# Kernel optimization log

Measured on AMD Instinct MI355X. Metric: run time of the kernel, lower is better.

Reference implementation:

```python
import jax, jax.numpy as jnp
import numpy as np

N, E, M, NT, RB, SH, NIR, LAT = 10000, 160000, 8, 4, 8, 9, 3, 128
AVG_N = 16.0
LATF = LAT + M * NIR  # 152
COMP2IR = np.array([0, 1, 1, 1, 2, 2, 2, 2, 2])  # irrep id per SH component (0e,1o,2e)
IR1H = jnp.asarray(np.eye(NIR, dtype=np.float32)[COMP2IR])  # [9,3] one-hot comp->irrep


def _silu(x):
    return x * jax.nn.sigmoid(x)


def setup_inputs() -> dict:
    key = jax.random.key(0)
    ks = jax.random.split(key, 16)
    def w(k, shape, fan_in):
        return jax.random.normal(k, shape, jnp.float32) / np.sqrt(fan_in)
    return {
        'edge_attrs': jax.random.normal(ks[0], (E, SH), jnp.float32),
        'edge_embedding': jax.random.normal(ks[1], (E, RB), jnp.float32),
        'node_attrs': jax.random.uniform(ks[2], (N, NT), jnp.float32),
        'edge_lengths': jax.random.uniform(ks[3], (E,), jnp.float32),
        'tb_w0': w(ks[4], (2 * NT + RB, LAT), 2 * NT + RB),
        'tb_w1': w(ks[5], (LAT, LAT), LAT),
        'tb_w2': w(ks[6], (LAT, LAT), LAT),
        'env_mlp_w0': w(ks[7], (LAT, 2 * M * NIR), LAT),
        'env_mlp_w1': w(ks[8], (LAT, M * NIR), LAT),
        'env_linear_w': w(ks[9], (2, NIR, M, M), M),
        'latent_w': w(ks[10], (LATF, LAT), LATF),
        'lat2feat_w': w(ks[11], (2, LATF, NIR * M * M), LATF),
        'lat2featold_w': w(ks[12], (2, LATF, NIR * M * M), LATF),
        'final_w': w(ks[13], (LATF, M), LATF),
        'edge_index': jax.random.randint(ks[14], (2, E), 0, N, jnp.int32),
    }


def reference(edge_attrs, edge_embedding, node_attrs, edge_lengths,
              tb_w0, tb_w1, tb_w2, env_mlp_w0, env_mlp_w1, env_linear_w,
              latent_w, lat2feat_w, lat2featold_w, final_w, edge_index):
    center, neigh = edge_index[0], edge_index[1]
    n_nodes = node_attrs.shape[0]
    c2i = jnp.asarray(COMP2IR)

    # polynomial cutoff, p=6, x = r / r_max
    x = edge_lengths
    p = 6.0
    cut = (1.0 - (p + 1) * (p + 2) / 2 * x**6 + p * (p + 2) * x**7 - p * (p + 1) / 2 * x**8)
    cut = jnp.where(x < 1.0, cut, 0.0)[:, None]

    # two-body latent MLP on [center species, neighbor species, radial basis]
    tb_in = jnp.concatenate([node_attrs[center], node_attrs[neigh], edge_embedding], axis=-1)
    h = _silu(tb_in @ tb_w0)
    h = _silu(h @ tb_w1)
    latents = (h @ tb_w2) * cut  # [E, LAT]

    def weight_edges(wch):  # MakeWeightedChannels: per-irrep channel weights
        return wch[:, :, c2i] * edge_attrs[:, None, :]  # [E, M, 9]

    def env_of(w_cur, layer):  # scatter to node env + env linear
        env = jax.ops.segment_sum(weight_edges(w_cur), center, num_segments=n_nodes) / AVG_N
        Wc = env_linear_w[layer][c2i]  # [9, M, M]
        return jnp.einsum('duv,nvd->nud', Wc, env) / np.sqrt(M)

    def interact(features, env_c):  # scalar-gated equivariant coupling
        return features * env_c[:, :, :1] + env_c * features[:, :, :1]

    def invariants(f):  # per-(channel, irrep) norms
        return jnp.sqrt(jnp.einsum('eud,di->eui', f * f, IR1H) + 1e-8).reshape(f.shape[0], M * NIR)

    def pe_linear(Wflat, f):  # per-edge generated irrep-wise Linear
        W = Wflat.reshape(-1, NIR, M, M)
        return jnp.einsum('eiuv,di,evd->eud', W, IR1H, f) / np.sqrt(M)

    # ---- layer 0 (initial weighter + env weighter) ----
    ew = latents @ env_mlp_w0  # [E, 2*M*NIR]
    w_init = ew[:, :M * NIR].reshape(-1, M, NIR)
    w_cur = ew[:, M * NIR:].reshape(-1, M, NIR)
    features = weight_edges(w_init)  # [E, M, 9]
    env_c = env_of(w_cur, 0)[center]
    new_f = interact(features, env_c)
    lat_full = jnp.concatenate([latents, invariants(new_f)], axis=-1)  # [E, 152]
    features = 0.5 * pe_linear(lat_full @ lat2featold_w[0], features) \
             + 0.5 * pe_linear(lat_full @ lat2feat_w[0], new_f)

    # ---- layer 1 ----
    lat_new = _silu(lat_full @ latent_w) * cut
    latents = 0.5 * latents + 0.5 * lat_new  # latent resnet, sigmoid(0)=0.5
    w_cur = (latents @ env_mlp_w1).reshape(-1, M, NIR)
    env_c = env_of(w_cur, 1)[center]
    new_f = interact(features, env_c)
    lat_full = jnp.concatenate([latents, invariants(new_f)], axis=-1)
    features = 0.5 * pe_linear(lat_full @ lat2featold_w[1], features) \
             + 0.5 * pe_linear(lat_full @ lat2feat_w[1], new_f)

    # ---- final: generated linear to 1x1o per edge (components 1:4) ----
    wfin = lat_full @ final_w  # [E, M]
    return jnp.einsum('em,emd->ed', wfin, features[:, :, 1:4]) / np.sqrt(M)
```

## Files before the change

kernel.cpp:

```cpp
#include <hip/hip_runtime.h>
#include <hip/hip_bf16.h>

#define EE 160000
#define NNODES 10000

using bf16 = __hip_bfloat16;
using bf16x8 = __attribute__((ext_vector_type(8))) short;
using short4v = __attribute__((ext_vector_type(4))) short;
using f32x4  = __attribute__((ext_vector_type(4))) float;

__device__ __forceinline__ float silu_f(float x) { return x / (1.0f + __expf(-x)); }
__device__ __forceinline__ float b2f(bf16 v) { return __bfloat162float(v); }
__device__ __forceinline__ bf16 f2b(float v) { return __float2bfloat16(v); }

__device__ __forceinline__ unsigned bfbits(float v) {
    union { float f; unsigned u; } a; a.f = v;
    return (a.u + 0x7fffu + ((a.u >> 16) & 1u)) >> 16;
}
__device__ __forceinline__ unsigned pack2(float a, float b) {
    return bfbits(a) | (bfbits(b) << 16);
}
__device__ __forceinline__ void unpack2(unsigned u, float& a, float& b) {
    union { unsigned x; float f; } lo, hi;
    lo.x = u << 16; hi.x = u & 0xffff0000u;
    a = lo.f; b = hi.f;
}
__device__ __forceinline__ float bs2f(short s) {
    union { unsigned u; float f; } x; x.u = ((unsigned)(unsigned short)s) << 16;
    return x.f;
}

#define INV_AVGN_SQM 0.02209708691207961f
#define HALF_INV_SQM 0.17677669529663687f
#define INV_SQM      0.35355339059327373f

__global__ void kCnt(const int* __restrict__ eidx, int* __restrict__ deg)
{
    const int e = blockIdx.x * 256 + threadIdx.x;
    atomicAdd(&deg[eidx[e]], 1);
}

__global__ void kScan(const int* __restrict__ deg, int* __restrict__ off)
{
    __shared__ int part[256];
    const int t = threadIdx.x;
    int loc[40];
    int s = 0;
#pragma unroll
    for (int i = 0; i < 40; i++) {
        const int idx = t * 40 + i;
        const int v = (idx < NNODES) ? deg[idx] : 0;
        loc[i] = s;
        s += v;
    }
    part[t] = s;
    __syncthreads();
    for (int d = 1; d < 256; d <<= 1) {
        const int v = (t >= d) ? part[t - d] : 0;
        __syncthreads();
        part[t] += v;
        __syncthreads();
    }
    const int base = (t == 0) ? 0 : part[t - 1];
#pragma unroll
    for (int i = 0; i < 40; i++) {
        const int idx = t * 40 + i;
        if (idx < NNODES) off[idx] = base + loc[i];
    }
    if (t == 255) off[NNODES] = part[255];
}

__global__ void kFill(const int* __restrict__ eidx, int* __restrict__ cur,
                      const int* __restrict__ off, int* __restrict__ elist)
{
    const int e = blockIdx.x * 256 + threadIdx.x;
    const int c = eidx[e];
    const int pos = atomicAdd(&cur[c], 1);
    elist[off[c] + pos] = e;
}

__global__ void kPrepA(const float* __restrict__ w1, const float* __restrict__ w2,
                       const float* __restrict__ wm0, short* __restrict__ wAtF)
{
    const int t = blockIdx.x * 256 + threadIdx.x;
    if (t >= 38912) return;
    const int k = t & 127, c = t >> 7;
    float v;
    if (c < 128)      v = w1[k * 128 + c];
    else if (c < 256) v = w2[k * 128 + (c - 128)];
    else              v = wm0[k * 48 + (c - 256)];
    wAtF[((k >> 3) * 304 + c) * 8 + (k & 7)] = (short)bfbits(v);
}

__global__ void kPrepB(const float* __restrict__ l2fo, const float* __restrict__ l2fn,
                       const float* __restrict__ latw, const float* __restrict__ l2fo1,
                       const float* __restrict__ l2fn1, const float* __restrict__ finw,
                       const float* __restrict__ wm1, short* __restrict__ BtF)
{
    const int k = blockIdx.y;
    const int col = blockIdx.x * 256 + threadIdx.x;
    if (col >= 672) return;
    float v = 0.f;
    if (col < 648) {
        if (k < 152) {
            if (col < 384) {
                const int ir = col >> 7, half = (col >> 6) & 1, q = col & 63;
                const float* src = half ? l2fn : l2fo;
                v = src[k * 192 + ir * 64 + q];
            } else if (col < 512)  v = latw[k * 128 + (col - 384)];
            else if (col < 576)    v = l2fo1[k * 192 + 64 + (col - 512)];
            else if (col < 640)    v = l2fn1[k * 192 + 64 + (col - 576)];
            else                   v = finw[k * 8 + (col - 640)];
        }
    } else {
        if (k < 128) v = wm1[k * 24 + (col - 648)];
    }
    BtF[((k >> 3) * 672 + col) * 8 + (k & 7)] = (short)bfbits(v);
}

__global__ void kEnvG(const float* __restrict__ wcur, const float* __restrict__ ea,
                      const int* __restrict__ off, const int* __restrict__ elist,
                      const float* __restrict__ wl, float* __restrict__ envc)
{
    const int t = blockIdx.x * 256 + threadIdx.x;
    if (t >= NNODES * 9) return;
    const int n = t / 9;
    const int d = t - n * 9;
    const int irr = (d == 0) ? 0 : ((d < 4) ? 1 : 2);
    float v[8];
#pragma unroll
    for (int q = 0; q < 8; q++) v[q] = 0.0f;
    const int b = off[n], en = off[n + 1];
    for (int j = b; j < en; j++) {
        const int e = elist[j];
        const float ad = ea[e * 9 + d];
        const float* wr = wcur + (size_t)e * 24 + irr;
#pragma unroll
        for (int q = 0; q < 8; q++) v[q] = fmaf(wr[q * 3], ad, v[q]);
    }
#pragma unroll
    for (int u = 0; u < 8; u++) {
        float s = 0.0f;
#pragma unroll
        for (int q = 0; q < 8; q++) s = fmaf(wl[irr * 64 + u * 8 + q], v[q], s);
        envc[n * 72 + u * 9 + d] = s * INV_AVGN_SQM;
    }
}

__global__ __launch_bounds__(256) void kA0(
    const float* __restrict__ ea, const float* __restrict__ eemb,
    const float* __restrict__ nat, const float* __restrict__ elen,
    const float* __restrict__ w0, const int* __restrict__ eidx,
    short* __restrict__ h08, short* __restrict__ latf8s,
    bf16* __restrict__ eaT, float* __restrict__ cutb)
{
    __shared__ float w0s[16 * 128];
    const int t = threadIdx.x;
    const int e = blockIdx.x * 256 + t;
#pragma unroll
    for (int p = 0; p < 8; p++) { const int idx = p * 256 + t; w0s[idx] = w0[idx]; }
    __syncthreads();

    const int ctr = eidx[e];
    const int ngb = eidx[EE + e];
    float tin[16];
#pragma unroll
    for (int k = 0; k < 4; k++) tin[k] = nat[ctr * 4 + k];
#pragma unroll
    for (int k = 0; k < 4; k++) tin[4 + k] = nat[ngb * 4 + k];
#pragma unroll
    for (int k = 0; k < 8; k++) tin[8 + k] = eemb[e * 8 + k];

    const float x = elen[e];
    const float x2 = x * x, x4 = x2 * x2, x6 = x4 * x2, x7 = x6 * x, x8 = x7 * x;
    float cutv = 1.0f - 28.0f * x6 + 48.0f * x7 - 21.0f * x8;
    cutv = (x < 1.0f) ? cutv : 0.0f;
    cutb[e] = cutv;

    const size_t tb = (size_t)(e >> 5);
    const int el = e & 31;
#pragma unroll
    for (int jc = 0; jc < 4; jc++) {
        float a[32];
#pragma unroll
        for (int j = 0; j < 32; j++) a[j] = 0.0f;
#pragma unroll
        for (int k = 0; k < 16; k++) {
            const float v = tin[k];
#pragma unroll
            for (int j = 0; j < 32; j++) a[j] = fmaf(v, w0s[k * 128 + jc * 32 + j], a[j]);
        }
#pragma unroll
        for (int cc = 0; cc < 4; cc++) {
            bf16x8 hv;
#pragma unroll
            for (int jj = 0; jj < 8; jj++) hv[jj] = (short)bfbits(silu_f(a[cc * 8 + jj]));
            *(bf16x8*)(h08 + tb * 4096 + (jc * 4 + cc) * 256 + el * 8) = hv;
        }
    }
    bf16x8 z;
#pragma unroll
    for (int jj = 0; jj < 8; jj++) z[jj] = 0;
    *(bf16x8*)(latf8s + tb * 5120 + 19 * 256 + el * 8) = z;

#pragma unroll
    for (int d = 0; d < 9; d++) eaT[(size_t)d * EE + e] = f2b(ea[e * 9 + d]);
}

__global__ __launch_bounds__(256, 4) void kAm(
    const short* __restrict__ h08, const short* __restrict__ wAtF,
    const float* __restrict__ cutb, short* __restrict__ latf8s,
    float* __restrict__ winiF, float* __restrict__ wcur0)
{
    __shared__ alignas(16) char a2raw[16384];
    __shared__ short A3[8192];
    short* A2 = (short*)a2raw;
    float* Cs = (float*)a2raw;

    const int t = threadIdx.x;
    const int eb = blockIdx.x * 64;
    const int lane = t & 63, wid = t >> 6;
    const int wm = wid >> 1, wn = wid & 1;
    const int l15 = lane & 15, kq = lane >> 4;
    const f32x4 zz = {0.f, 0.f, 0.f, 0.f};

    float cutR[2][4];
#pragma unroll
    for (int mi = 0; mi < 2; mi++)
#pragma unroll
        for (int r = 0; r < 4; r++)
            cutR[mi][r] = cutb[eb + wm * 32 + mi * 16 + kq * 4 + r];

    {
        f32x4 acc[8];
#pragma unroll
        for (int q = 0; q < 8; q++) acc[q] = zz;
        const size_t ab = (size_t)((eb >> 5) + wm) * 4096 + l15 * 8;
#pragma unroll
        for (int ks = 0; ks < 4; ks++) {
            const int kc = ks * 4 + kq;
            const bf16x8 a0 = *(const bf16x8*)(h08 + ab + kc * 256);
            const bf16x8 a1 = *(const bf16x8*)(h08 + ab + kc * 256 + 128);
            const short* bp = wAtF + (kc * 304 + wn * 64 + l15) * 8;
#pragma unroll
            for (int ni = 0; ni < 4; ni++) {
                const bf16x8 b = *(const bf16x8*)(bp + ni * 16 * 8);
                acc[ni]     = __builtin_amdgcn_mfma_f32_16x16x32_bf16(a0, b, acc[ni], 0, 0, 0);
                acc[4 + ni] = __builtin_amdgcn_mfma_f32_16x16x32_bf16(a1, b, acc[4 + ni], 0, 0, 0);
            }
        }
#pragma unroll
        for (int mi = 0; mi < 2; mi++)
#pragma unroll
            for (int ni = 0; ni < 4; ni++) {
                const int kcol = wn * 64 + ni * 16 + l15;
                const int eb2 = wm * 32 + mi * 16 + (kq << 2);
#pragma unroll
                for (int r = 0; r < 4; r++)
                    A2[(kcol >> 3) * 512 + (eb2 + r) * 8 + (kcol & 7)] =
                        (short)bfbits(silu_f(acc[mi * 4 + ni][r]));
            }
    }
    __syncthreads();

    {
        f32x4 acc[8];
#pragma unroll
        for (int q = 0; q < 8; q++) acc[q] = zz;
#pragma unroll
        for (int ks = 0; ks < 4; ks++) {
            const int kc = ks * 4 + kq;
            const bf16x8 a0 = *(const bf16x8*)(A2 + kc * 512 + (wm * 32 + l15) * 8);
            const bf16x8 a1 = *(const bf16x8*)(A2 + kc * 512 + (wm * 32 + 16 + l15) * 8);
            const short* bp = wAtF + (kc * 304 + 128 + wn * 64 + l15) * 8;
#pragma unroll
            for (int ni = 0; ni < 4; ni++) {
                const bf16x8 b = *(const bf16x8*)(bp + ni * 16 * 8);
                acc[ni]     = __builtin_amdgcn_mfma_f32_16x16x32_bf16(a0, b, acc[ni], 0, 0, 0);
                acc[4 + ni] = __builtin_amdgcn_mfma_f32_16x16x32_bf16(a1, b, acc[4 + ni], 0, 0, 0);
            }
        }
#pragma unroll
        for (int mi = 0; mi < 2; mi++)
#pragma unroll
            for (int ni = 0; ni < 4; ni++) {
                const int kcol = wn * 64 + ni * 16 + l15;
                const int eb2 = wm * 32 + mi * 16 + (kq << 2);
#pragma unroll
                for (int r = 0; r < 4; r++)
                    A3[(kcol >> 3) * 512 + (eb2 + r) * 8 + (kcol & 7)] =
                        (short)bfbits(acc[mi * 4 + ni][r] * cutR[mi][r]);
            }
    }
    __syncthreads();
#pragma unroll
    for (int p = 0; p < 4; p++) {
        const int i = p * 256 + t;
        const int e = i & 63, kc = i >> 6;
        const bf16x8 v = *(const bf16x8*)(A3 + kc * 512 + e * 8);
        const int eg = eb + e;
        *(bf16x8*)(latf8s + (size_t)(eg >> 5) * 5120 + kc * 256 + (eg & 31) * 8) = v;
    }

    if (wn == 0) {
        f32x4 acc[6];
#pragma unroll
        for (int q = 0; q < 6; q++) acc[q] = zz;
#pragma unroll
        for (int ks = 0; ks < 4; ks++) {
            const int kc = ks * 4 + kq;
            const bf16x8 a0 = *(const bf16x8*)(A3 + kc * 512 + (wm * 32 + l15) * 8);
            const bf16x8 a1 = *(const bf16x8*)(A3 + kc * 512 + (wm * 32 + 16 + l15) * 8);
            const short* bp = wAtF + (kc * 304 + 256 + l15) * 8;
#pragma unroll
            for (int ni = 0; ni < 3; ni++) {
                const bf16x8 b = *(const bf16x8*)(bp + ni * 16 * 8);
                acc[ni]     = __builtin_amdgcn_mfma_f32_16x16x32_bf16(a0, b, acc[ni], 0, 0, 0);
                acc[3 + ni] = __builtin_amdgcn_mfma_f32_16x16x32_bf16(a1, b, acc[3 + ni], 0, 0, 0);
            }
        }
#pragma unroll
        for (int mi = 0; mi < 2; mi++)
#pragma unroll
            for (int ni = 0; ni < 3; ni++) {
                const int c = ni * 16 + l15;
                const int eb2 = wm * 32 + mi * 16 + (kq << 2);
#pragma unroll
                for (int r = 0; r < 4; r++)
                    Cs[c * 65 + eb2 + r] = acc[mi * 3 + ni][r];
            }
    }
    __syncthreads();
    for (int i = t; i < 1536; i += 256) {
        const int c = i >> 6, e = i & 63;
        winiF[(size_t)c * EE + eb + e] = Cs[c * 65 + e];
    }
    for (int i = t; i < 1536; i += 256) {
        const int e2 = i / 24, c2 = i - e2 * 24;
        wcur0[(size_t)(eb + e2) * 24 + c2] = Cs[(24 + c2) * 65 + e2];
    }
}

__global__ __launch_bounds__(256, 1) void kC1(
    const float* __restrict__ winiF, const bf16* __restrict__ eaT,
    const float* __restrict__ envc, const int* __restrict__ eidx,
    unsigned* __restrict__ newfT, short* __restrict__ latf8s)
{
    const int e = blockIdx.x * 256 + threadIdx.x;
    const int ctr = eidx[e];
    float eav[9];
#pragma unroll
    for (int d = 0; d < 9; d++) eav[d] = b2f(eaT[(size_t)d * EE + e]);
    const float* ec = envc + ctr * 72;
    float inv[24];
#pragma unroll
    for (int uh = 0; uh < 4; uh++) {
        const int u0 = 2 * uh;
        float wi0[3], wi1[3];
#pragma unroll
        for (int i = 0; i < 3; i++) {
            wi0[i] = winiF[(size_t)(u0 * 3 + i) * EE + e];
            wi1[i] = winiF[(size_t)((u0 + 1) * 3 + i) * EE + e];
        }
        float nf0[9], nf1[9];
        const float ec00 = ec[u0 * 9 + 0];
        const float ec10 = ec[(u0 + 1) * 9 + 0];
        const float f00 = wi0[0] * eav[0];
        const float f10 = wi1[0] * eav[0];
#pragma unroll
        for (int d = 0; d < 9; d++) {
            const int irr = (d == 0) ? 0 : ((d < 4) ? 1 : 2);
            const float fa = wi0[irr] * eav[d];
            const float fb = wi1[irr] * eav[d];
            nf0[d] = fa * ec00 + ec[u0 * 9 + d] * f00;
            nf1[d] = fb * ec10 + ec[(u0 + 1) * 9 + d] * f10;
        }
#pragma unroll
        for (int d = 0; d < 9; d++) newfT[(size_t)(d * 4 + uh) * EE + e] = pack2(nf0[d], nf1[d]);
        inv[uh * 6 + 0] = sqrtf(nf0[0] * nf0[0] + 1e-8f);
        inv[uh * 6 + 1] = sqrtf(nf0[1]*nf0[1] + nf0[2]*nf0[2] + nf0[3]*nf0[3] + 1e-8f);
        inv[uh * 6 + 2] = sqrtf(nf0[4]*nf0[4] + nf0[5]*nf0[5] + nf0[6]*nf0[6] + nf0[7]*nf0[7] + nf0[8]*nf0[8] + 1e-8f);
        inv[uh * 6 + 3] = sqrtf(nf1[0] * nf1[0] + 1e-8f);
        inv[uh * 6 + 4] = sqrtf(nf1[1]*nf1[1] + nf1[2]*nf1[2] + nf1[3]*nf1[3] + 1e-8f);
        inv[uh * 6 + 5] = sqrtf(nf1[4]*nf1[4] + nf1[5]*nf1[5] + nf1[6]*nf1[6] + nf1[7]*nf1[7] + nf1[8]*nf1[8] + 1e-8f);
    }
    const size_t tb = (size_t)(e >> 5);
    const int el = e & 31;
#pragma unroll
    for (int j = 0; j < 3; j++) {
        bf16x8 iv;
#pragma unroll
        for (int jj = 0; jj < 8; jj++) iv[jj] = (short)bfbits(inv[j * 8 + jj]);
        *(bf16x8*)(latf8s + tb * 5120 + (16 + j) * 256 + el * 8) = iv;
    }
}

__global__ __launch_bounds__(256, 4) void kF0(
    const short* __restrict__ A8, const short* __restrict__ BtF,
    const float* __restrict__ winiF, const bf16* __restrict__ eaT,
    const unsigned* __restrict__ newfT, unsigned* __restrict__ feat1T)
{
    __shared__ float Cs[128 * 67];
    const int t = threadIdx.x;
    const int eb = blockIdx.x * 64;
    const int lane = t & 63, wid = t >> 6;
    const int wm = wid >> 1, wn = wid & 1;
    const int l15 = lane & 15, kq = lane >> 4;
    const f32x4 zz = {0.f, 0.f, 0.f, 0.f};
    const size_t ab = (size_t)((eb >> 5) + wm) * 5120 + l15 * 8;
    const int te = t & 63, uh = t >> 6;
    const int eg = eb + te;

    for (int ir = 0; ir < 3; ir++) {
        f32x4 acc[8];
#pragma unroll
        for (int q = 0; q < 8; q++) acc[q] = zz;
#pragma unroll
        for (int ks = 0; ks < 5; ks++) {
            const int kc = ks * 4 + kq;
            const bf16x8 a0 = *(const bf16x8*)(A8 + ab + kc * 256);
            const bf16x8 a1 = *(const bf16x8*)(A8 + ab + kc * 256 + 128);
            const short* bp = BtF + (kc * 672 + ir * 128 + wn * 64 + l15) * 8;
#pragma unroll
            for (int ni = 0; ni < 4; ni++) {
                const bf16x8 b = *(const bf16x8*)(bp + ni * 16 * 8);
                acc[ni]     = __builtin_amdgcn_mfma_f32_16x16x32_bf16(a0, b, acc[ni], 0, 0, 0);
                acc[4 + ni] = __builtin_amdgcn_mfma_f32_16x16x32_bf16(a1, b, acc[4 + ni], 0, 0, 0);
            }
        }
        __syncthreads();
#pragma unroll
        for (int mi = 0; mi < 2; mi++)
#pragma unroll
            for (int ni = 0; ni < 4; ni++) {
                const int cl = wn * 64 + ni * 16 + l15;
                const int el = wm * 32 + mi * 16 + (kq << 2);
                const f32x4 v = acc[mi * 4 + ni];
#pragma unroll
                for (int r = 0; r < 4; r++) Cs[cl * 67 + el + r] = v[r];
            }
        __syncthreads();
        const int d0 = (ir == 0) ? 0 : ((ir == 1) ? 1 : 4);
        const int nd = (ir == 0) ? 1 : ((ir == 1) ? 3 : 5);
        float wv[8];
#pragma unroll
        for (int v8 = 0; v8 < 8; v8++) wv[v8] = winiF[(size_t)(v8 * 3 + ir) * EE + eg];
        for (int dd = 0; dd < nd; dd++) {
            const int d = d0 + dd;
            const float ead = b2f(eaT[(size_t)d * EE + eg]);
            float nfv[8];
#pragma unroll
            for (int q = 0; q < 4; q++)
                unpack2(newfT[(size_t)(d * 4 + q) * EE + eg], nfv[2 * q], nfv[2 * q + 1]);
            float s0 = 0.f, s1 = 0.f;
#pragma unroll
            for (int v8 = 0; v8 < 8; v8++) {
                const float fe = wv[v8] * ead;
                s0 += Cs[(uh * 16 + v8) * 67 + te] * fe + Cs[(64 + uh * 16 + v8) * 67 + te] * nfv[v8];
                s1 += Cs[(uh * 16 + 8 + v8) * 67 + te] * fe + Cs[(64 + uh * 16 + 8 + v8) * 67 + te] * nfv[v8];
            }
            feat1T[(size_t)(d * 4 + uh) * EE + eg] = pack2(s0 * HALF_INV_SQM, s1 * HALF_INV_SQM);
        }
    }
}

__global__ __launch_bounds__(256, 4) void kF3(
    short* __restrict__ A8, const short* __restrict__ BtF,
    const float* __restrict__ cutb, float* __restrict__ wcur1)
{
    __shared__ alignas(16) short Cc[128 * 68];
    __shared__ short l1s[16 * 512];
    float* Cw = (float*)Cc;
    const int t = threadIdx.x;
    const int eb = blockIdx.x * 64;
    const int lane = t & 63, wid = t >> 6;
    const int wm = wid >> 1, wn = wid & 1;
    const int l15 = lane & 15, kq = lane >> 4;
    const f32x4 zz = {0.f, 0.f, 0.f, 0.f};

    {
        f32x4 acc[8];
#pragma unroll
        for (int q = 0; q < 8; q++) acc[q] = zz;
        const size_t ab = (size_t)((eb >> 5) + wm) * 5120 + l15 * 8;
#pragma unroll
        for (int ks = 0; ks < 5; ks++) {
            const int kc = ks * 4 + kq;
            const bf16x8 a0 = *(const bf16x8*)(A8 + ab + kc * 256);
            const bf16x8 a1 = *(const bf16x8*)(A8 + ab + kc * 256 + 128);
            const short* bp = BtF + (kc * 672 + 384 + wn * 64 + l15) * 8;
#pragma unroll
            for (int ni = 0; ni < 4; ni++) {
                const bf16x8 b = *(const bf16x8*)(bp + ni * 16 * 8);
                acc[ni]     = __builtin_amdgcn_mfma_f32_16x16x32_bf16(a0, b, acc[ni], 0, 0, 0);
                acc[4 + ni] = __builtin_amdgcn_mfma_f32_16x16x32_bf16(a1, b, acc[4 + ni], 0, 0, 0);
            }
        }
#pragma unroll
        for (int mi = 0; mi < 2; mi++)
#pragma unroll
            for (int ni = 0; ni < 4; ni++) {
                const int cl = wn * 64 + ni * 16 + l15;
                const int el = wm * 32 + mi * 16 + (kq << 2);
                const f32x4 v = acc[mi * 4 + ni];
                short4v pv;
#pragma unroll
                for (int r = 0; r < 4; r++) pv[r] = (short)bfbits(v[r]);
                *(short4v*)(Cc + cl * 68 + el) = pv;
            }
    }
    __syncthreads();
    {
        const int te = t & 63, q = t >> 6;
        const int eg = eb + te;
        const size_t tb = (size_t)(eg >> 5);
        const int el2 = eg & 31;
        const float cutv = cutb[eg];
#pragma unroll
        for (int c = 0; c < 4; c++) {
            const int kc = q * 4 + c;
            short* ap = A8 + tb * 5120 + kc * 256 + el2 * 8;
            const bf16x8 ov = *(const bf16x8*)ap;
            bf16x8 nv;
#pragma unroll
            for (int jj = 0; jj < 8; jj++) {
                const int j = kc * 8 + jj;
                const float g = bs2f(Cc[j * 68 + te]);
                const float o = bs2f(ov[jj]);
                nv[jj] = (short)bfbits(0.5f * o + 0.5f * silu_f(g) * cutv);
            }
            *(bf16x8*)ap = nv;
            *(bf16x8*)(l1s + kc * 512 + te * 8) = nv;
        }
    }
    __syncthreads();
    if (wn == 0) {
        f32x4 acc[4] = {zz, zz, zz, zz};
#pragma unroll
        for (int ks = 0; ks < 4; ks++) {
            const int kc = ks * 4 + kq;
            const bf16x8 a0 = *(const bf16x8*)(l1s + kc * 512 + (wm * 32 + l15) * 8);
            const bf16x8 a1 = *(const bf16x8*)(l1s + kc * 512 + (wm * 32 + 16 + l15) * 8);
#pragma unroll
            for (int ni = 0; ni < 2; ni++) {
                const int c = ni * 16 + l15;
                bf16x8 b;
                if (c < 24) b = *(const bf16x8*)(BtF + (kc * 672 + 648 + c) * 8);
                else {
#pragma unroll
                    for (int jj = 0; jj < 8; jj++) b[jj] = 0;
                }
                acc[ni]     = __builtin_amdgcn_mfma_f32_16x16x32_bf16(a0, b, acc[ni], 0, 0, 0);
                acc[2 + ni] = __builtin_amdgcn_mfma_f32_16x16x32_bf16(a1, b, acc[2 + ni], 0, 0, 0);
            }
        }
#pragma unroll
        for (int mi = 0; mi < 2; mi++)
#pragma unroll
            for (int ni = 0; ni < 2; ni++) {
                const int c = ni * 16 + l15;
                if (c < 24) {
                    const int el = wm * 32 + mi * 16 + (kq << 2);
#pragma unroll
                    for (int r = 0; r < 4; r++) Cw[c * 65 + el + r] = acc[mi * 2 + ni][r];
                }
            }
    }
    __syncthreads();
    for (int i = t; i < 1536; i += 256) {
        const int e2 = i / 24, c2 = i - e2 * 24;
        wcur1[(size_t)(eb + e2) * 24 + c2] = Cw[c2 * 65 + e2];
    }
}

__global__ __launch_bounds__(256, 1) void kE1(
    const unsigned* __restrict__ feat1T, const float* __restrict__ envc,
    const int* __restrict__ eidx, unsigned* __restrict__ newfT,
    short* __restrict__ latf8s)
{
    const int e = blockIdx.x * 256 + threadIdx.x;
    const int ctr = eidx[e];
    const float* ec = envc + ctr * 72;
    float inv[24];
#pragma unroll
    for (int uh = 0; uh < 4; uh++) {
        const int u0 = 2 * uh;
        float f0[9], f1[9];
#pragma unroll
        for (int d = 0; d < 9; d++) unpack2(feat1T[(size_t)(d * 4 + uh) * EE + e], f0[d], f1[d]);
        const float ec00 = ec[u0 * 9 + 0];
        const float ec10 = ec[(u0 + 1) * 9 + 0];
        float nf0[9], nf1[9];
#pragma unroll
        for (int d = 0; d < 9; d++) {
            nf0[d] = f0[d] * ec00 + ec[u0 * 9 + d] * f0[0];
            nf1[d] = f1[d] * ec10 + ec[(u0 + 1) * 9 + d] * f1[0];
        }
#pragma unroll
        for (int d = 0; d < 9; d++) newfT[(size_t)(d * 4 + uh) * EE + e] = pack2(nf0[d], nf1[d]);
        inv[uh * 6 + 0] = sqrtf(nf0[0] * nf0[0] + 1e-8f);
        inv[uh * 6 + 1] = sqrtf(nf0[1]*nf0[1] + nf0[2]*nf0[2] + nf0[3]*nf0[3] + 1e-8f);
        inv[uh * 6 + 2] = sqrtf(nf0[4]*nf0[4] + nf0[5]*nf0[5] + nf0[6]*nf0[6] + nf0[7]*nf0[7] + nf0[8]*nf0[8] + 1e-8f);
        inv[uh * 6 + 3] = sqrtf(nf1[0] * nf1[0] + 1e-8f);
        inv[uh * 6 + 4] = sqrtf(nf1[1]*nf1[1] + nf1[2]*nf1[2] + nf1[3]*nf1[3] + 1e-8f);
        inv[uh * 6 + 5] = sqrtf(nf1[4]*nf1[4] + nf1[5]*nf1[5] + nf1[6]*nf1[6] + nf1[7]*nf1[7] + nf1[8]*nf1[8] + 1e-8f);
    }
    const size_t tb = (size_t)(e >> 5);
    const int el = e & 31;
#pragma unroll
    for (int j = 0; j < 3; j++) {
        bf16x8 iv;
#pragma unroll
        for (int jj = 0; jj < 8; jj++) iv[jj] = (short)bfbits(inv[j * 8 + jj]);
        *(bf16x8*)(latf8s + tb * 5120 + (16 + j) * 256 + el * 8) = iv;
    }
}

__global__ __launch_bounds__(256, 4) void kF2(
    const short* __restrict__ A8, const short* __restrict__ BtF,
    const unsigned* __restrict__ feat1T, const unsigned* __restrict__ newfT,
    float* __restrict__ outp)
{
    __shared__ float Cs[128 * 67];
    __shared__ float Cwf[16 * 67];
    const int t = threadIdx.x;
    const int eb = blockIdx.x * 64;
    const int lane = t & 63, wid = t >> 6;
    const int wm = wid >> 1, wn = wid & 1;
    const int l15 = lane & 15, kq = lane >> 4;
    const f32x4 zz = {0.f, 0.f, 0.f, 0.f};
    const size_t ab = (size_t)((eb >> 5) + wm) * 5120 + l15 * 8;

    {
        f32x4 acc[8];
#pragma unroll
        for (int q = 0; q < 8; q++) acc[q] = zz;
#pragma unroll
        for (int ks = 0; ks < 5; ks++) {
            const int kc = ks * 4 + kq;
            const bf16x8 a0 = *(const bf16x8*)(A8 + ab + kc * 256);
            const bf16x8 a1 = *(const bf16x8*)(A8 + ab + kc * 256 + 128);
            const short* bp = BtF + (kc * 672 + 512 + wn * 64 + l15) * 8;
#pragma unroll
            for (int ni = 0; ni < 4; ni++) {
                const bf16x8 b = *(const bf16x8*)(bp + ni * 16 * 8);
                acc[ni]     = __builtin_amdgcn_mfma_f32_16x16x32_bf16(a0, b, acc[ni], 0, 0, 0);
                acc[4 + ni] = __builtin_amdgcn_mfma_f32_16x16x32_bf16(a1, b, acc[4 + ni], 0, 0, 0);
            }
        }
#pragma unroll
        for (int mi = 0; mi < 2; mi++)
#pragma unroll
            for (int ni = 0; ni < 4; ni++) {
                const int cl = wn * 64 + ni * 16 + l15;
                const int el = wm * 32 + mi * 16 + (kq << 2);
                const f32x4 v = acc[mi * 4 + ni];
#pragma unroll
                for (int r = 0; r < 4; r++) Cs[cl * 67 + el + r] = v[r];
            }
    }
    {
        f32x4 a2[2] = {zz, zz};
        bf16x8 bz;
#pragma unroll
        for (int jj = 0; jj < 8; jj++) bz[jj] = 0;
#pragma unroll
        for (int ks = 0; ks < 5; ks++) {
            const int kc = ks * 4 + kq;
            const bf16x8 a0 = *(const bf16x8*)(A8 + ab + kc * 256);
            const bf16x8 a1 = *(const bf16x8*)(A8 + ab + kc * 256 + 128);
            const bf16x8 b = (l15 < 8)
                ? *(const bf16x8*)(BtF + (kc * 672 + 640 + l15) * 8) : bz;
            a2[0] = __builtin_amdgcn_mfma_f32_16x16x32_bf16(a0, b, a2[0], 0, 0, 0);
            a2[1] = __builtin_amdgcn_mfma_f32_16x16x32_bf16(a1, b, a2[1], 0, 0, 0);
        }
        if (wn == 0) {
#pragma unroll
            for (int mi = 0; mi < 2; mi++) {
                const int el = wm * 32 + mi * 16 + (kq << 2);
#pragma unroll
                for (int r = 0; r < 4; r++) Cwf[l15 * 67 + el + r] = a2[mi][r];
            }
        }
    }
    __syncthreads();
    if (t < 192) {
        const int te = t % 64;
        const int dd = t / 64;
        const int eg = eb + te;
        const int d = 1 + dd;
        float f1v[8], nfv[8];
#pragma unroll
        for (int q = 0; q < 4; q++) {
            unpack2(feat1T[(size_t)(d * 4 + q) * EE + eg], f1v[2 * q], f1v[2 * q + 1]);
            unpack2(newfT[(size_t)(d * 4 + q) * EE + eg], nfv[2 * q], nfv[2 * q + 1]);
        }
        float od = 0.f;
#pragma unroll
        for (int u = 0; u < 8; u++) {
            float s = 0.f;
#pragma unroll
            for (int v8 = 0; v8 < 8; v8++)
                s += Cs[(u * 8 + v8) * 67 + te] * f1v[v8] + Cs[(64 + u * 8 + v8) * 67 + te] * nfv[v8];
            od = fmaf(Cwf[u * 67 + te], s, od);
        }
        outp[(size_t)eg * 3 + dd] = od * (HALF_INV_SQM * INV_SQM);
    }
}

extern "C" void kernel_launch(void* const* d_in, const int* in_sizes, int n_in,
                              void* d_out, int out_size, void* d_ws, size_t ws_size,
                              hipStream_t stream)
{
    const float* ea   = (const float*)d_in[0];
    const float* eemb = (const float*)d_in[1];
    const float* nat  = (const float*)d_in[2];
    const float* elen = (const float*)d_in[3];
    const float* w0   = (const float*)d_in[4];
    const float* w1   = (const float*)d_in[5];
    const float* w2   = (const float*)d_in[6];
    const float* wm0  = (const float*)d_in[7];
    const float* wm1  = (const float*)d_in[8];
    const float* envl = (const float*)d_in[9];
    const float* latw = (const float*)d_in[10];
    const float* l2fn = (const float*)d_in[11];
    const float* l2fo = (const float*)d_in[12];
    const float* finw = (const float*)d_in[13];
    const int*   eidx = (const int*)d_in[14];

    char* ws = (char*)d_ws;
    short*    latf8s = (short*)(ws + 0);
    short*    h08    = (short*)(ws + 51200000);
    unsigned* newfT  = (unsigned*)(ws + 92160000);
    unsigned* feat1T = (unsigned*)(ws + 115200000);
    float*    winiF  = (float*)(ws + 138240000);
    bf16*     eaT    = (bf16*)(ws + 153600000);
    float*    cutb   = (float*)(ws + 156480000);
    float*    env0   = (float*)(ws + 157120000);
    float*    env1   = (float*)(ws + 160000000);
    int*      deg    = (int*)(ws + 162880000);
    int*      cur    = (int*)(ws + 162920000);
    int*      off    = (int*)(ws + 162960000);
    int*      elist  = (int*)(ws + 163000192);
    short*    wAtF   = (short*)(ws + 162880000);
    short*    BtF    = (short*)(ws + 163640192);

    float* wcur0 = (float*)newfT;
    float* wcur1 = (float*)newfT;

    hipMemsetAsync(deg, 0, 80000, stream);

    kCnt <<<625, 256, 0, stream>>>(eidx, deg);
    kScan<<<1, 256, 0, stream>>>(deg, off);
    kFill<<<625, 256, 0, stream>>>(eidx, cur, off, elist);
    kPrepA<<<152, 256, 0, stream>>>(w1, w2, wm0, wAtF);
    kPrepB<<<dim3(3, 160), 256, 0, stream>>>(l2fo, l2fn, latw,
                                             l2fo + 29184, l2fn + 29184, finw, wm1, BtF);

    kA0<<<625, 256, 0, stream>>>(ea, eemb, nat, elen, w0, eidx, h08, latf8s, eaT, cutb);
    kAm<<<2500, 256, 0, stream>>>(h08, wAtF, cutb, latf8s, winiF, wcur0);
    kEnvG<<<352, 256, 0, stream>>>(wcur0, ea, off, elist, envl + 0, env0);
    kC1<<<625, 256, 0, stream>>>(winiF, eaT, env0, eidx, newfT, latf8s);

    kF0<<<2500, 256, 0, stream>>>(latf8s, BtF, winiF, eaT, newfT, feat1T);
    kF3<<<2500, 256, 0, stream>>>(latf8s, BtF, cutb, wcur1);
    kEnvG<<<352, 256, 0, stream>>>(wcur1, ea, off, elist, envl + 192, env1);
    kE1<<<625, 256, 0, stream>>>(feat1T, env1, eidx, newfT, latf8s);
    kF2<<<2500, 256, 0, stream>>>(latf8s, BtF, feat1T, newfT, (float*)d_out);
}
```

Before: 313.3 us.

## Fuse kF0 and kF3 into one kernel sharing register-cached A fragments

Merges the layer-0 feature-update GEMM kernel and the latent-update kernel into a single kernel. The A-operand fragments of the 152-wide latent row are loaded once into registers and reused across four column chunks. This removes one launch and one full re-read of the latent tile. The same A-fragment hoisting is applied in kF2. wcur1 is redirected to the h08 buffer because newfT is still read while wcur1 is being written in the fused kernel. In exchange, register pressure rises from holding 10 bf16x8 fragments, and the second GEMM now rereads updated latents from global memory instead of LDS.

After: 343.0 us. +9.4%, slower.

```diff
diff --git a/kernel.cpp b/kernel.cpp
--- a/kernel.cpp
+++ b/kernel.cpp
@@ -395,12 +395,14 @@
     }
 }
 
-__global__ __launch_bounds__(256, 4) void kF0(
-    const short* __restrict__ A8, const short* __restrict__ BtF,
+__global__ __launch_bounds__(256, 4) void kFX(
+    short* __restrict__ A8, const short* __restrict__ BtF,
     const float* __restrict__ winiF, const bf16* __restrict__ eaT,
-    const unsigned* __restrict__ newfT, unsigned* __restrict__ feat1T)
+    const unsigned* __restrict__ newfT, const float* __restrict__ cutb,
+    unsigned* __restrict__ feat1T, float* __restrict__ wcur1)
 {
     __shared__ float Cs[128 * 67];
+    float* Cw = Cs;
     const int t = threadIdx.x;
     const int eb = blockIdx.x * 64;
     const int lane = t & 63, wid = t >> 6;
@@ -411,21 +413,27 @@
     const int te = t & 63, uh = t >> 6;
     const int eg = eb + te;
 
-    for (int ir = 0; ir < 3; ir++) {
+    bf16x8 aF0[5], aF1[5];
+#pragma unroll
+    for (int ks = 0; ks < 5; ks++) {
+        const int kc = ks * 4 + kq;
+        aF0[ks] = *(const bf16x8*)(A8 + ab + kc * 256);
+        aF1[ks] = *(const bf16x8*)(A8 + ab + kc * 256 + 128);
+    }
+
+    for (int c = 0; c < 4; c++) {
         f32x4 acc[8];
 #pragma unroll
         for (int q = 0; q < 8; q++) acc[q] = zz;
 #pragma unroll
         for (int ks = 0; ks < 5; ks++) {
             const int kc = ks * 4 + kq;
-            const bf16x8 a0 = *(const bf16x8*)(A8 + ab + kc * 256);
-            const bf16x8 a1 = *(const bf16x8*)(A8 + ab + kc * 256 + 128);
-            const short* bp = BtF + (kc * 672 + ir * 128 + wn * 64 + l15) * 8;
+            const short* bp = BtF + (kc * 672 + c * 128 + wn * 64 + l15) * 8;
 #pragma unroll
             for (int ni = 0; ni < 4; ni++) {
                 const bf16x8 b = *(const bf16x8*)(bp + ni * 16 * 8);
-                acc[ni]     = __builtin_amdgcn_mfma_f32_16x16x32_bf16(a0, b, acc[ni], 0, 0, 0);
-                acc[4 + ni] = __builtin_amdgcn_mfma_f32_16x16x32_bf16(a1, b, acc[4 + ni], 0, 0, 0);
+                acc[ni]     = __builtin_amdgcn_mfma_f32_16x16x32_bf16(aF0[ks], b, acc[ni], 0, 0, 0);
+                acc[4 + ni] = __builtin_amdgcn_mfma_f32_16x16x32_bf16(aF1[ks], b, acc[4 + ni], 0, 0, 0);
             }
         }
         __syncthreads();
@@ -440,129 +448,79 @@
                 for (int r = 0; r < 4; r++) Cs[cl * 67 + el + r] = v[r];
             }
         __syncthreads();
-        const int d0 = (ir == 0) ? 0 : ((ir == 1) ? 1 : 4);
-        const int nd = (ir == 0) ? 1 : ((ir == 1) ? 3 : 5);
-        float wv[8];
-#pragma unroll
-        for (int v8 = 0; v8 < 8; v8++) wv[v8] = winiF[(size_t)(v8 * 3 + ir) * EE + eg];
-        for (int dd = 0; dd < nd; dd++) {
-            const int d = d0 + dd;
-            const float ead = b2f(eaT[(size_t)d * EE + eg]);
-            float nfv[8];
-#pragma unroll
-            for (int q = 0; q < 4; q++)
-                unpack2(newfT[(size_t)(d * 4 + q) * EE + eg], nfv[2 * q], nfv[2 * q + 1]);
-            float s0 = 0.f, s1 = 0.f;
-#pragma unroll
-            for (int v8 = 0; v8 < 8; v8++) {
-                const float fe = wv[v8] * ead;
-                s0 += Cs[(uh * 16 + v8) * 67 + te] * fe + Cs[(64 + uh * 16 + v8) * 67 + te] * nfv[v8];
-                s1 += Cs[(uh * 16 + 8 + v8) * 67 + te] * fe + Cs[(64 + uh * 16 + 8 + v8) * 67 + te] * nfv[v8];
-            }
-            feat1T[(size_t)(d * 4 + uh) * EE + eg] = pack2(s0 * HALF_INV_SQM, s1 * HALF_INV_SQM);
-        }
-    }
-}
-
-__global__ __launch_bounds__(256, 4) void kF3(
-    short* __restrict__ A8, const short* __restrict__ BtF,
-    const float* __restrict__ cutb, float* __restrict__ wcur1)
-{
-    __shared__ alignas(16) short Cc[128 * 68];
-    __shared__ short l1s[16 * 512];
-    float* Cw = (float*)Cc;
-    const int t = threadIdx.x;
-    const int eb = blockIdx.x * 64;
-    const int lane = t & 63, wid = t >> 6;
-    const int wm = wid >> 1, wn = wid & 1;
-    const int l15 = lane & 15, kq = lane >> 4;
-    const f32x4 zz = {0.f, 0.f, 0.f, 0.f};
-
-    {
-        f32x4 acc[8];
-#pragma unroll
-        for (int q = 0; q < 8; q++) acc[q] = zz;
-        const size_t ab = (size_t)((eb >> 5) + wm) * 5120 + l15 * 8;
-#pragma unroll
-        for (int ks = 0; ks < 5; ks++) {
+        if (c < 3) {
+            const int ir = c;
+            const int d0 = (ir == 0) ? 0 : ((ir == 1) ? 1 : 4);
+            const int nd = (ir == 0) ? 1 : ((ir == 1) ? 3 : 5);
+            float wv[8];
+#pragma unroll
+            for (int v8 = 0; v8 < 8; v8++) wv[v8] = winiF[(size_t)(v8 * 3 + ir) * EE + eg];
+            for (int dd = 0; dd < nd; dd++) {
+                const int d = d0 + dd;
+                const float ead = b2f(eaT[(size_t)d * EE + eg]);
+                float nfv[8];
+#pragma unroll
+                for (int q = 0; q < 4; q++)
+                    unpack2(newfT[(size_t)(d * 4 + q) * EE + eg], nfv[2 * q], nfv[2 * q + 1]);
+                float s0 = 0.f, s1 = 0.f;
+#pragma unroll
+                for (int v8 = 0; v8 < 8; v8++) {
+                    const float fe = wv[v8] * ead;
+                    s0 += Cs[(uh * 16 + v8) * 67 + te] * fe + Cs[(64 + uh * 16 + v8) * 67 + te] * nfv[v8];
+                    s1 += Cs[(uh * 16 + 8 + v8) * 67 + te] * fe + Cs[(64 + uh * 16 + 8 + v8) * 67 + te] * nfv[v8];
+                }
+                feat1T[(size_t)(d * 4 + uh) * EE + eg] = pack2(s0 * HALF_INV_SQM, s1 * HALF_INV_SQM);
+            }
+        } else {
+            const size_t tbq = (size_t)(eg >> 5);
+            const int el2 = eg & 31;
+            const float cutv = cutb[eg];
+#pragma unroll
+            for (int cc2 = 0; cc2 < 4; cc2++) {
+                const int kc = uh * 4 + cc2;
+                short* ap = A8 + tbq * 5120 + kc * 256 + el2 * 8;
+                const bf16x8 ov = *(const bf16x8*)ap;
+                bf16x8 nv;
+#pragma unroll
+                for (int jj = 0; jj < 8; jj++) {
+                    const float g = Cs[(kc * 8 + jj) * 67 + te];
+                    const float o = bs2f(ov[jj]);
+                    nv[jj] = (short)bfbits(0.5f * o + 0.5f * silu_f(g) * cutv);
+                }
+                *(bf16x8*)ap = nv;
+            }
+        }
+    }
+    __syncthreads();
+    if (wn == 0) {
+        f32x4 acc4[4] = {zz, zz, zz, zz};
+#pragma unroll
+        for (int ks = 0; ks < 4; ks++) {
             const int kc = ks * 4 + kq;
             const bf16x8 a0 = *(const bf16x8*)(A8 + ab + kc * 256);
             const bf16x8 a1 = *(const bf16x8*)(A8 + ab + kc * 256 + 128);
-            const short* bp = BtF + (kc * 672 + 384 + wn * 64 + l15) * 8;
-#pragma unroll
-            for (int ni = 0; ni < 4; ni++) {
-                const bf16x8 b = *(const bf16x8*)(bp + ni * 16 * 8);
-                acc[ni]     = __builtin_amdgcn_mfma_f32_16x16x32_bf16(a0, b, acc[ni], 0, 0, 0);
-                acc[4 + ni] = __builtin_amdgcn_mfma_f32_16x16x32_bf16(a1, b, acc[4 + ni], 0, 0, 0);
-            }
-        }
-#pragma unroll
-        for (int mi = 0; mi < 2; mi++)
-#pragma unroll
-            for (int ni = 0; ni < 4; ni++) {
-                const int cl = wn * 64 + ni * 16 + l15;
-                const int el = wm * 32 + mi * 16 + (kq << 2);
-                const f32x4 v = acc[mi * 4 + ni];
-                short4v pv;
-#pragma unroll
-                for (int r = 0; r < 4; r++) pv[r] = (short)bfbits(v[r]);
-                *(short4v*)(Cc + cl * 68 + el) = pv;
-            }
-    }
-    __syncthreads();
-    {
-        const int te = t & 63, q = t >> 6;
-        const int eg = eb + te;
-        const size_t tb = (size_t)(eg >> 5);
-        const int el2 = eg & 31;
-        const float cutv = cutb[eg];
-#pragma unroll
-        for (int c = 0; c < 4; c++) {
-            const int kc = q * 4 + c;
-            short* ap = A8 + tb * 5120 + kc * 256 + el2 * 8;
-            const bf16x8 ov = *(const bf16x8*)ap;
-            bf16x8 nv;
-#pragma unroll
-            for (int jj = 0; jj < 8; jj++) {
-                const int j = kc * 8 + jj;
-                const float g = bs2f(Cc[j * 68 + te]);
-                const float o = bs2f(ov[jj]);
-                nv[jj] = (short)bfbits(0.5f * o + 0.5f * silu_f(g) * cutv);
-            }
-            *(bf16x8*)ap = nv;
-            *(bf16x8*)(l1s + kc * 512 + te * 8) = nv;
-        }
-    }
-    __syncthreads();
-    if (wn == 0) {
-        f32x4 acc[4] = {zz, zz, zz, zz};
-#pragma unroll
-        for (int ks = 0; ks < 4; ks++) {
-            const int kc = ks * 4 + kq;
-            const bf16x8 a0 = *(const bf16x8*)(l1s + kc * 512 + (wm * 32 + l15) * 8);
-            const bf16x8 a1 = *(const bf16x8*)(l1s + kc * 512 + (wm * 32 + 16 + l15) * 8);
 #pragma unroll
             for (int ni = 0; ni < 2; ni++) {
-                const int c = ni * 16 + l15;
+                const int cc = ni * 16 + l15;
                 bf16x8 b;
-                if (c < 24) b = *(const bf16x8*)(BtF + (kc * 672 + 648 + c) * 8);
+                if (cc < 24) b = *(const bf16x8*)(BtF + (kc * 672 + 648 + cc) * 8);
                 else {
 #pragma unroll
                     for (int jj = 0; jj < 8; jj++) b[jj] = 0;
                 }
-                acc[ni]     = __builtin_amdgcn_mfma_f32_16x16x32_bf16(a0, b, acc[ni], 0, 0, 0);
-                acc[2 + ni] = __builtin_amdgcn_mfma_f32_16x16x32_bf16(a1, b, acc[2 + ni], 0, 0, 0);
+                acc4[ni]     = __builtin_amdgcn_mfma_f32_16x16x32_bf16(a0, b, acc4[ni], 0, 0, 0);
+                acc4[2 + ni] = __builtin_amdgcn_mfma_f32_16x16x32_bf16(a1, b, acc4[2 + ni], 0, 0, 0);
             }
         }
 #pragma unroll
         for (int mi = 0; mi < 2; mi++)
 #pragma unroll
             for (int ni = 0; ni < 2; ni++) {
-                const int c = ni * 16 + l15;
-                if (c < 24) {
+                const int cc = ni * 16 + l15;
+                if (cc < 24) {
                     const int el = wm * 32 + mi * 16 + (kq << 2);
 #pragma unroll
-                    for (int r = 0; r < 4; r++) Cw[c * 65 + el + r] = acc[mi * 2 + ni][r];
+                    for (int r = 0; r < 4; r++) Cw[cc * 65 + el + r] = acc4[mi * 2 + ni][r];
                 }
             }
     }
@@ -631,6 +589,14 @@
     const f32x4 zz = {0.f, 0.f, 0.f, 0.f};
     const size_t ab = (size_t)((eb >> 5) + wm) * 5120 + l15 * 8;
 
+    bf16x8 aF0[5], aF1[5];
+#pragma unroll
+    for (int ks = 0; ks < 5; ks++) {
+        const int kc = ks * 4 + kq;
+        aF0[ks] = *(const bf16x8*)(A8 + ab + kc * 256);
+        aF1[ks] = *(const bf16x8*)(A8 + ab + kc * 256 + 128);
+    }
+
     {
         f32x4 acc[8];
 #pragma unroll
@@ -638,14 +604,12 @@
 #pragma unroll
         for (int ks = 0; ks < 5; ks++) {
             const int kc = ks * 4 + kq;
-            const bf16x8 a0 = *(const bf16x8*)(A8 + ab + kc * 256);
-            const bf16x8 a1 = *(const bf16x8*)(A8 + ab + kc * 256 + 128);
             const short* bp = BtF + (kc * 672 + 512 + wn * 64 + l15) * 8;
 #pragma unroll
             for (int ni = 0; ni < 4; ni++) {
                 const bf16x8 b = *(const bf16x8*)(bp + ni * 16 * 8);
-                acc[ni]     = __builtin_amdgcn_mfma_f32_16x16x32_bf16(a0, b, acc[ni], 0, 0, 0);
-                acc[4 + ni] = __builtin_amdgcn_mfma_f32_16x16x32_bf16(a1, b, acc[4 + ni], 0, 0, 0);
+                acc[ni]     = __builtin_amdgcn_mfma_f32_16x16x32_bf16(aF0[ks], b, acc[ni], 0, 0, 0);
+                acc[4 + ni] = __builtin_amdgcn_mfma_f32_16x16x32_bf16(aF1[ks], b, acc[4 + ni], 0, 0, 0);
             }
         }
 #pragma unroll
@@ -667,12 +631,10 @@
 #pragma unroll
         for (int ks = 0; ks < 5; ks++) {
             const int kc = ks * 4 + kq;
-            const bf16x8 a0 = *(const bf16x8*)(A8 + ab + kc * 256);
-            const bf16x8 a1 = *(const bf16x8*)(A8 + ab + kc * 256 + 128);
             const bf16x8 b = (l15 < 8)
                 ? *(const bf16x8*)(BtF + (kc * 672 + 640 + l15) * 8) : bz;
-            a2[0] = __builtin_amdgcn_mfma_f32_16x16x32_bf16(a0, b, a2[0], 0, 0, 0);
-            a2[1] = __builtin_amdgcn_mfma_f32_16x16x32_bf16(a1, b, a2[1], 0, 0, 0);
+            a2[0] = __builtin_amdgcn_mfma_f32_16x16x32_bf16(aF0[ks], b, a2[0], 0, 0, 0);
+            a2[1] = __builtin_amdgcn_mfma_f32_16x16x32_bf16(aF1[ks], b, a2[1], 0, 0, 0);
         }
         if (wn == 0) {
 #pragma unroll
@@ -746,7 +708,7 @@
     short*    BtF    = (short*)(ws + 163640192);
 
     float* wcur0 = (float*)newfT;
-    float* wcur1 = (float*)newfT;
+    float* wcur1 = (float*)h08;
 
     hipMemsetAsync(deg, 0, 80000, stream);
 
@@ -762,8 +724,7 @@
     kEnvG<<<352, 256, 0, stream>>>(wcur0, ea, off, elist, envl + 0, env0);
     kC1<<<625, 256, 0, stream>>>(winiF, eaT, env0, eidx, newfT, latf8s);
 
-    kF0<<<2500, 256, 0, stream>>>(latf8s, BtF, winiF, eaT, newfT, feat1T);
-    kF3<<<2500, 256, 0, stream>>>(latf8s, BtF, cutb, wcur1);
+    kFX<<<2500, 256, 0, stream>>>(latf8s, BtF, winiF, eaT, newfT, cutb, feat1T, wcur1);
     kEnvG<<<352, 256, 0, stream>>>(wcur1, ea, off, elist, envl + 192, env1);
     kE1<<<625, 256, 0, stream>>>(feat1T, env1, eidx, newfT, latf8s);
     kF2<<<2500, 256, 0, stream>>>(latf8s, BtF, feat1T, newfT, (float*)d_out);
```
